# Kernel tuning notes

Measured on AMD Instinct MI355X. Metric: run time of the kernel, lower is better.

## Reference

```python
import jax, jax.numpy as jnp
import numpy as np

N = 50000
E = 800000
F_IN = 128
HID = 64
HEADS = 4
P = 16384


def setup_inputs() -> dict:
    key = jax.random.key(0)
    ks = jax.random.split(key, 20)
    s = 0.05
    inp = {
        'x': jax.random.normal(ks[0], (N, F_IN), jnp.float32),
        'edge_src': jax.random.randint(ks[1], (E,), 0, N, jnp.int32),
        'edge_dst': jax.random.randint(ks[2], (E,), 0, N, jnp.int32),
        'edge_attr': jax.random.uniform(ks[3], (E, 1), jnp.float32),
        'pair_indices': jax.random.randint(ks[4], (P, 2), 0, N, jnp.int32),
        # conv1: in=F_IN, heads=4, out=HID, edge_dim=1
        'W1': jax.random.normal(ks[5], (F_IN, HEADS * HID), jnp.float32) * s,
        'We1': jax.random.normal(ks[6], (1, HEADS * HID), jnp.float32) * s,
        'as1': jax.random.normal(ks[7], (HEADS, HID), jnp.float32) * s,
        'ad1': jax.random.normal(ks[8], (HEADS, HID), jnp.float32) * s,
        'ae1': jax.random.normal(ks[9], (HEADS, HID), jnp.float32) * s,
        'b1': jnp.zeros((HEADS * HID,), jnp.float32),
        # conv2: in=4*HID, heads=1, out=HID
        'W2': jax.random.normal(ks[10], (HEADS * HID, HID), jnp.float32) * s,
        'We2': jax.random.normal(ks[11], (1, HID), jnp.float32) * s,
        'as2': jax.random.normal(ks[12], (1, HID), jnp.float32) * s,
        'ad2': jax.random.normal(ks[13], (1, HID), jnp.float32) * s,
        'ae2': jax.random.normal(ks[14], (1, HID), jnp.float32) * s,
        'b2': jnp.zeros((HID,), jnp.float32),
        'Wlin': jax.random.normal(ks[15], (2 * HID, 1), jnp.float32) * s,
        'blin': jnp.zeros((1,), jnp.float32),
    }
    return inp


def gat_conv(x, src, dst, edge_attr, W, We, att_src, att_dst, att_edge, bias, heads, C):
    """PyG GATConv (add_self_loops=True, fill_value='mean', negative_slope=0.2, eval mode)."""
    n = x.shape[0]
    # self-loop edge_attr = mean of incoming edge attrs per node
    deg = jax.ops.segment_sum(jnp.ones_like(dst, dtype=edge_attr.dtype), dst, num_segments=n)
    loop_attr = jax.ops.segment_sum(edge_attr, dst, num_segments=n) / jnp.maximum(deg, 1.0)[:, None]
    loop = jnp.arange(n, dtype=src.dtype)
    src_f = jnp.concatenate([src, loop])
    dst_f = jnp.concatenate([dst, loop])
    ea = jnp.concatenate([edge_attr, loop_attr], axis=0)  # [E+N, 1]
    h = (x @ W).reshape(n, heads, C)                      # [N, H, C]
    a_src = (h * att_src).sum(-1)                         # [N, H]
    a_dst = (h * att_dst).sum(-1)
    e = (ea @ We).reshape(-1, heads, C)                   # [E+N, H, C]
    a_edge = (e * att_edge).sum(-1)                       # [E+N, H]
    alpha = jax.nn.leaky_relu(a_src[src_f] + a_dst[dst_f] + a_edge, 0.2)
    amax = jax.ops.segment_max(alpha, dst_f, num_segments=n)
    ex = jnp.exp(alpha - amax[dst_f])
    denom = jax.ops.segment_sum(ex, dst_f, num_segments=n)
    w = ex / denom[dst_f]                                 # segment softmax over dst
    msg = h[src_f] * w[..., None]                         # [E+N, H, C]
    out = jax.ops.segment_sum(msg, dst_f, num_segments=n) # [N, H, C]
    return out.reshape(n, heads * C) + bias


def reference(x, edge_src, edge_dst, edge_attr, pair_indices,
              W1, We1, as1, ad1, ae1, b1,
              W2, We2, as2, ad2, ae2, b2, Wlin, blin):
    # dropout is identity in eval mode
    h1 = jax.nn.elu(gat_conv(x, edge_src, edge_dst, edge_attr,
                             W1, We1, as1, ad1, ae1, b1, HEADS, HID))
    h2 = gat_conv(h1, edge_src, edge_dst, edge_attr,
                  W2, We2, as2, ad2, ae2, b2, 1, HID)
    d1 = h2[pair_indices[:, 0]]
    d2 = h2[pair_indices[:, 1]]
    pf = jnp.concatenate([d1, d2], axis=1)                # [P, 2*HID]
    return jax.nn.sigmoid(pf @ Wlin + blin).reshape(-1)
```

## Files before the change

### kernel.cpp

```cpp
#include <hip/hip_runtime.h>
#include <hip/hip_fp16.h>
#include <math.h>

typedef __attribute__((ext_vector_type(8))) short short8;
typedef __attribute__((ext_vector_type(4))) float floatx4;
typedef __attribute__((ext_vector_type(2))) float float2v;

__device__ __forceinline__ unsigned short f2bf(float f){
  unsigned int x = __float_as_uint(f);
  unsigned int r = x + 0x7fff + ((x >> 16) & 1);
  return (unsigned short)(r >> 16);
}
__device__ __forceinline__ unsigned char f2fp8(float v){
  int pk = __builtin_amdgcn_cvt_pk_fp8_f32(v, 0.f, 0, false);
  return (unsigned char)(pk & 0xff);
}
__device__ __forceinline__ float wsumf(float v){
#pragma unroll
  for (int o = 32; o; o >>= 1) v += __shfl_xor(v, o, 64);
  return v;
}

__global__ __launch_bounds__(256) void k_count(const int* __restrict__ dst,
    const float* __restrict__ eattr, unsigned long long* __restrict__ degp,
    int* __restrict__ rank, int E, int N){
  int e = blockIdx.x * 256 + threadIdx.x;
  if (e >= E) return;
  int b = blockIdx.x & 7;
  int d = dst[e];
  unsigned long long add = (1ull << 40) |
      (unsigned long long)(eattr[e] * 16777216.0f);
  unsigned long long old = atomicAdd(&degp[(size_t)b * N + d], add);
  rank[e] = (int)(old >> 40);
}

__global__ __launch_bounds__(256) void k_scan1(const unsigned long long* __restrict__ degp,
    int* __restrict__ row_ptr, int* __restrict__ bsum, int n){
  __shared__ int sm[2][256];
  int tid = threadIdx.x, gid = blockIdx.x * 256 + tid;
  int v = 0;
  if (gid < n){
#pragma unroll
    for (int b = 0; b < 8; b++) v += (int)(degp[(size_t)b * n + gid] >> 40);
  }
  sm[0][tid] = v; __syncthreads();
  int pin = 0;
  for (int off = 1; off < 256; off <<= 1){
    int t = sm[pin][tid];
    if (tid >= off) t += sm[pin][tid - off];
    sm[pin ^ 1][tid] = t; pin ^= 1; __syncthreads();
  }
  int incl = sm[pin][tid];
  if (gid < n) row_ptr[gid] = incl - v;
  if (tid == 255) bsum[blockIdx.x] = incl;
}

__global__ __launch_bounds__(256) void k_scan2(const int* __restrict__ bsum,
    int* __restrict__ bofs, int nb){
  __shared__ int sm[2][256];
  int tid = threadIdx.x;
  int v = (tid < nb) ? bsum[tid] : 0;
  sm[0][tid] = v; __syncthreads();
  int pin = 0;
  for (int off = 1; off < 256; off <<= 1){
    int t = sm[pin][tid];
    if (tid >= off) t += sm[pin][tid - off];
    sm[pin ^ 1][tid] = t; pin ^= 1; __syncthreads();
  }
  bofs[tid] = sm[pin][tid] - v;
}

__global__ __launch_bounds__(256) void k_scan3(int* __restrict__ row_ptr,
    const int* __restrict__ bofs, const unsigned long long* __restrict__ degp,
    float* __restrict__ lattr, int* __restrict__ base, int n, int E){
  int gid = blockIdx.x * 256 + threadIdx.x;
  if (gid >= n) return;
  int rp = row_ptr[gid] + bofs[gid >> 8];
  row_ptr[gid] = rp;
  const unsigned long long M40 = (1ull << 40) - 1;
  int cum = 0; float s = 0.f;
  int bb[8];
#pragma unroll
  for (int b = 0; b < 8; b++){
    unsigned long long p = degp[(size_t)b * n + gid];
    bb[b] = rp + cum;
    cum += (int)(p >> 40);
    s += (float)(p & M40);
  }
  lattr[gid] = (s * (1.0f / 16777216.0f)) / fmaxf((float)cum, 1.0f);
  int4* bp = (int4*)(base + (size_t)gid * 8);
  bp[0] = make_int4(bb[0], bb[1], bb[2], bb[3]);
  bp[1] = make_int4(bb[4], bb[5], bb[6], bb[7]);
  if (gid == 0) row_ptr[n] = E;
}

__global__ __launch_bounds__(256) void k_scatter(const int* __restrict__ src,
    const int* __restrict__ dst, const float* __restrict__ eattr,
    const int* __restrict__ rank, const int* __restrict__ base,
    int2* __restrict__ csr, int E){
  int e = blockIdx.x * 256 + threadIdx.x;
  if (e >= E) return;
  int b = blockIdx.x & 7;
  int d = dst[e];
  int pos = base[(size_t)d * 8 + b] + rank[e];
  csr[pos] = make_int2(src[e], __float_as_int(eattr[e]));
}

__global__ void k_prep(const float* __restrict__ W1, const float* __restrict__ as1,
    const float* __restrict__ ad1, const float* __restrict__ W2,
    const float* __restrict__ as2, const float* __restrict__ ad2,
    const float* __restrict__ We1, const float* __restrict__ ae1,
    const float* __restrict__ We2, const float* __restrict__ ae2,
    unsigned short* __restrict__ W1p, unsigned short* __restrict__ W2p,
    float* __restrict__ ce){
  int b = blockIdx.x, lane = threadIdx.x;
  if (b < 68){
    int nt = b >> 2, kc = b & 3;
    int col = lane & 15, krow = kc * 32 + (lane >> 4) * 8;
    unsigned short tmp[8];
    if (nt < 16){
#pragma unroll
      for (int j = 0; j < 8; j++) tmp[j] = f2bf(W1[(size_t)(krow + j) * 256 + nt * 16 + col]);
    } else {
#pragma unroll
      for (int j = 0; j < 8; j++){
        float v = 0.f;
        if (col < 8){
          const float* av = (col < 4) ? as1 : ad1;
          int h = col & 3;
          for (int c = 0; c < 64; c++)
            v += W1[(size_t)(krow + j) * 256 + h * 64 + c] * av[h * 64 + c];
        }
        tmp[j] = f2bf(v);
      }
    }
    unsigned short* dstp = W1p + (((size_t)nt * 4 + kc) * 64 + lane) * 8;
    *(ushort4*)(dstp)     = make_ushort4(tmp[0], tmp[1], tmp[2], tmp[3]);
    *(ushort4*)(dstp + 4) = make_ushort4(tmp[4], tmp[5], tmp[6], tmp[7]);
  } else if (b < 108){
    int bb = b - 68;
    int nt = bb >> 3, kc = bb & 7;
    int col = lane & 15, krow = kc * 32 + (lane >> 4) * 8;
    unsigned short tmp[8];
    if (nt < 4){
#pragma unroll
      for (int j = 0; j < 8; j++) tmp[j] = f2bf(W2[(size_t)(krow + j) * 64 + nt * 16 + col]);
    } else {
#pragma unroll
      for (int j = 0; j < 8; j++){
        float v = 0.f;
        if (col < 2){
          const float* av = (col == 0) ? as2 : ad2;
          for (int c = 0; c < 64; c++)
            v += W2[(size_t)(krow + j) * 64 + c] * av[c];
        }
        tmp[j] = f2bf(v);
      }
    }
    unsigned short* dstp = W2p + (((size_t)nt * 8 + kc) * 64 + lane) * 8;
    *(ushort4*)(dstp)     = make_ushort4(tmp[0], tmp[1], tmp[2], tmp[3]);
    *(ushort4*)(dstp + 4) = make_ushort4(tmp[4], tmp[5], tmp[6], tmp[7]);
  } else {
    float p0 = We1[lane]       * ae1[lane];
    float p1 = We1[64 + lane]  * ae1[64 + lane];
    float p2 = We1[128 + lane] * ae1[128 + lane];
    float p3 = We1[192 + lane] * ae1[192 + lane];
    float p4 = We2[lane]       * ae2[lane];
    p0 = wsumf(p0); p1 = wsumf(p1); p2 = wsumf(p2); p3 = wsumf(p3); p4 = wsumf(p4);
    if (lane == 0){ ce[0] = p0; ce[1] = p1; ce[2] = p2; ce[3] = p3; ce[4] = p4; }
  }
}

__global__ __launch_bounds__(256) void k_gemm1_att(const float* __restrict__ A,
    const unsigned short* __restrict__ Bp, unsigned char* __restrict__ h1f8,
    float* __restrict__ asrc, float* __restrict__ adst, int M){
  constexpr int K = 128, NKC = 4;
  __shared__ unsigned short Bs[256 * K];
  {
    const uint4* srcp = (const uint4*)Bp;
    uint4* dstp = (uint4*)Bs;
    for (int i = threadIdx.x; i < 4096; i += 256) dstp[i] = srcp[i];
  }
  __syncthreads();
  int wave = threadIdx.x >> 6, lane = threadIdx.x & 63;
  int quad = lane >> 4, col = lane & 15;
  int r0 = (blockIdx.x * 4 + wave) * 16;
  int rowc = min(r0 + col, M - 1);
  short8 af[NKC], sf[NKC];
#pragma unroll
  for (int kc = 0; kc < NKC; kc++){
    float4 a0 = *(const float4*)(A + (size_t)rowc * K + kc * 32 + quad * 8);
    float4 a1 = *(const float4*)(A + (size_t)rowc * K + kc * 32 + quad * 8 + 4);
    short8 t;
    t[0] = (short)f2bf(a0.x); t[1] = (short)f2bf(a0.y);
    t[2] = (short)f2bf(a0.z); t[3] = (short)f2bf(a0.w);
    t[4] = (short)f2bf(a1.x); t[5] = (short)f2bf(a1.y);
    t[6] = (short)f2bf(a1.z); t[7] = (short)f2bf(a1.w);
    af[kc] = t;
    sf[kc] = *(const short8*)(Bp + (((size_t)16 * 4 + kc) * 64 + lane) * 8);
  }
  floatx4 acc[17];
#pragma unroll
  for (int nt = 0; nt < 17; nt++) acc[nt] = (floatx4){0.f, 0.f, 0.f, 0.f};
#pragma unroll
  for (int kc = 0; kc < NKC; kc++){
#pragma unroll
    for (int nt = 0; nt < 16; nt++){
      short8 bfv = *(const short8*)(&Bs[((nt * NKC + kc) * 64 + lane) * 8]);
      acc[nt] = __builtin_amdgcn_mfma_f32_16x16x32_bf16(af[kc], bfv, acc[nt], 0, 0, 0);
    }
    acc[16] = __builtin_amdgcn_mfma_f32_16x16x32_bf16(af[kc], sf[kc], acc[16], 0, 0, 0);
  }
#pragma unroll
  for (int nt = 0; nt < 16; nt++){
#pragma unroll
    for (int i = 0; i < 4; i++){
      int r = r0 + quad * 4 + i;
      if (r < M) h1f8[(size_t)r * 256 + nt * 16 + col] = f2fp8(acc[nt][i]);
    }
  }
#pragma unroll
  for (int i = 0; i < 4; i++){
    int r = r0 + quad * 4 + i;
    if (r < M){
      float v = acc[16][i];
      if (col < 4)      asrc[(size_t)r * 4 + col] = v;
      else if (col < 8) adst[(size_t)r * 4 + (col - 4)] = v;
    }
  }
}

__global__ __launch_bounds__(256) void k_gemm2_att(const unsigned short* __restrict__ A,
    const unsigned short* __restrict__ Bp, unsigned char* __restrict__ h2f8,
    float* __restrict__ asrc, float* __restrict__ adst, int M){
  constexpr int K = 256, NKC = 8;
  __shared__ unsigned short Bs[64 * K];
  {
    const uint4* srcp = (const uint4*)Bp;
    uint4* dstp = (uint4*)Bs;
    for (int i = threadIdx.x; i < 2048; i += 256) dstp[i] = srcp[i];
  }
  __syncthreads();
  int wave = threadIdx.x >> 6, lane = threadIdx.x & 63;
  int quad = lane >> 4, col = lane & 15;
  int r0 = (blockIdx.x * 4 + wave) * 16;
  int rowc = min(r0 + col, M - 1);
  short8 af[NKC], sf[NKC];
#pragma unroll
  for (int kc = 0; kc < NKC; kc++){
    af[kc] = *(const short8*)(A + (size_t)rowc * K + kc * 32 + quad * 8);
    sf[kc] = *(const short8*)(Bp + (((size_t)4 * 8 + kc) * 64 + lane) * 8);
  }
  floatx4 acc[5];
#pragma unroll
  for (int nt = 0; nt < 5; nt++) acc[nt] = (floatx4){0.f, 0.f, 0.f, 0.f};
#pragma unroll
  for (int kc = 0; kc < NKC; kc++){
#pragma unroll
    for (int nt = 0; nt < 4; nt++){
      short8 bfv = *(const short8*)(&Bs[((nt * NKC + kc) * 64 + lane) * 8]);
      acc[nt] = __builtin_amdgcn_mfma_f32_16x16x32_bf16(af[kc], bfv, acc[nt], 0, 0, 0);
    }
    acc[4] = __builtin_amdgcn_mfma_f32_16x16x32_bf16(af[kc], sf[kc], acc[4], 0, 0, 0);
  }
#pragma unroll
  for (int nt = 0; nt < 4; nt++){
#pragma unroll
    for (int i = 0; i < 4; i++){
      int r = r0 + quad * 4 + i;
      if (r < M) h2f8[(size_t)r * 64 + nt * 16 + col] = f2fp8(acc[nt][i]);
    }
  }
#pragma unroll
  for (int i = 0; i < 4; i++){
    int r = r0 + quad * 4 + i;
    if (r < M){
      float v = acc[4][i];
      if (col == 0)      asrc[r] = v;
      else if (col == 1) adst[r] = v;
    }
  }
}

__global__ __launch_bounds__(256) void k_gat1(
    const int* __restrict__ row_ptr, const int2* __restrict__ csr,
    const float* __restrict__ lattr,
    const float* __restrict__ a_src, const float* __restrict__ a_dst,
    const float* __restrict__ ce, const unsigned char* __restrict__ hpre,
    const float* __restrict__ bias, unsigned short* __restrict__ hout, int n){
  int node = blockIdx.x * 4 + (threadIdx.x >> 6);
  if (node >= n) return;
  int lane = threadIdx.x & 63;
  int q = lane >> 4, lsub = lane & 15, hq = lsub >> 2;
  int start = row_ptr[node], deg = row_ptr[node + 1] - start;
  float4 as4 = *(const float4*)(a_src + (size_t)node * 4);
  float4 ad4 = *(const float4*)(a_dst + (size_t)node * 4);
  float4 ce4 = *(const float4*)ce;
  float la = lattr[node];
  float asvh = hq == 0 ? as4.x : hq == 1 ? as4.y : hq == 2 ? as4.z : as4.w;
  float advh = hq == 0 ? ad4.x : hq == 1 ? ad4.y : hq == 2 ? ad4.z : ad4.w;
  float ceh  = hq == 0 ? ce4.x : hq == 1 ? ce4.y : hq == 2 ? ce4.z : ce4.w;
  float2v acc2[8];
#pragma unroll
  for (int k = 0; k < 8; k++) acc2[k] = (float2v){0.f, 0.f};
  float dn = 0.f;
  if (q == 0){
    float aself = asvh + advh + la * ceh;
    aself = aself > 0.f ? aself : 0.2f * aself;
    float wself = __expf(aself);
    dn = wself;
    uint4 u = *(const uint4*)(hpre + (size_t)node * 256 + lsub * 16);
    float2v w2 = (float2v){wself, wself};
    unsigned uu[4] = {u.x, u.y, u.z, u.w};
#pragma unroll
    for (int j = 0; j < 4; j++){
      acc2[2 * j]     = w2 * __builtin_amdgcn_cvt_pk_f32_fp8((int)uu[j], false);
      acc2[2 * j + 1] = w2 * __builtin_amdgcn_cvt_pk_f32_fp8((int)uu[j], true);
    }
  }
  for (int e = q; e < deg; e += 8){
    bool vB = (e + 4) < deg;
    int2 seA = csr[start + e];
    int2 seB = csr[start + (vB ? e + 4 : e)];
    float aA = a_src[(size_t)seA.x * 4 + hq] + advh + __int_as_float(seA.y) * ceh;
    aA = aA > 0.f ? aA : 0.2f * aA;
    float wA = __expf(aA);
    float aB = a_src[(size_t)seB.x * 4 + hq] + advh + __int_as_float(seB.y) * ceh;
    aB = aB > 0.f ? aB : 0.2f * aB;
    float wB = vB ? __expf(aB) : 0.f;
    uint4 uA = *(const uint4*)(hpre + (size_t)seA.x * 256 + lsub * 16);
    uint4 uB = *(const uint4*)(hpre + (size_t)seB.x * 256 + lsub * 16);
    dn += wA + wB;
    float2v wA2 = (float2v){wA, wA}, wB2 = (float2v){wB, wB};
    unsigned ua[4] = {uA.x, uA.y, uA.z, uA.w};
    unsigned ub[4] = {uB.x, uB.y, uB.z, uB.w};
#pragma unroll
    for (int j = 0; j < 4; j++){
      acc2[2 * j]     += wA2 * __builtin_amdgcn_cvt_pk_f32_fp8((int)ua[j], false);
      acc2[2 * j + 1] += wA2 * __builtin_amdgcn_cvt_pk_f32_fp8((int)ua[j], true);
      acc2[2 * j]     += wB2 * __builtin_amdgcn_cvt_pk_f32_fp8((int)ub[j], false);
      acc2[2 * j + 1] += wB2 * __builtin_amdgcn_cvt_pk_f32_fp8((int)ub[j], true);
    }
  }
  dn += __shfl_xor(dn, 16, 64);
  dn += __shfl_xor(dn, 32, 64);
#pragma unroll
  for (int k = 0; k < 8; k++){
    acc2[k].x += __shfl_xor(acc2[k].x, 16, 64);
    acc2[k].x += __shfl_xor(acc2[k].x, 32, 64);
    acc2[k].y += __shfl_xor(acc2[k].y, 16, 64);
    acc2[k].y += __shfl_xor(acc2[k].y, 32, 64);
  }
  if (q == 0){
    float inv = 1.f / dn;
    float bb[16];
#pragma unroll
    for (int j = 0; j < 4; j++){
      float4 b4 = *(const float4*)(bias + lsub * 16 + j * 4);
      bb[j * 4 + 0] = b4.x; bb[j * 4 + 1] = b4.y;
      bb[j * 4 + 2] = b4.z; bb[j * 4 + 3] = b4.w;
    }
    unsigned short o[16];
#pragma unroll
    for (int k = 0; k < 16; k++){
      float av = (k & 1) ? acc2[k >> 1].y : acc2[k >> 1].x;
      float v = av * inv + bb[k];
      v = v > 0.f ? v : (__expf(v) - 1.f);
      o[k] = f2bf(v);
    }
    unsigned short* op = hout + (size_t)node * 256 + lsub * 16;
    *(uint4*)(op)     = *(uint4*)(o);
    *(uint4*)(op + 8) = *(uint4*)(o + 8);
  }
}

__global__ __launch_bounds__(256) void k_gat2(
    const int* __restrict__ row_ptr, const int2* __restrict__ csr,
    const float* __restrict__ lattr,
    const float* __restrict__ a_src, const float* __restrict__ a_dst,
    const float* __restrict__ ce, const unsigned char* __restrict__ hpre,
    const float* __restrict__ bias, const float* __restrict__ Wlin,
    float* __restrict__ s1v, float* __restrict__ s2v, int n){
  int node = blockIdx.x * 4 + (threadIdx.x >> 6);
  if (node >= n) return;
  int lane = threadIdx.x & 63;
  int slot = lane >> 3, lsub = lane & 7;
  int start = row_ptr[node], deg = row_ptr[node + 1] - start;
  float adn = a_dst[node], c = ce[4];
  float2v acc2[4];
#pragma unroll
  for (int k = 0; k < 4; k++) acc2[k] = (float2v){0.f, 0.f};
  float dn = 0.f;
  if (slot == 0){
    float aself = a_src[node] + adn + lattr[node] * c;
    aself = aself > 0.f ? aself : 0.2f * aself;
    float wself = __expf(aself);
    dn = wself;
    uint2 u = *(const uint2*)(hpre + (size_t)node * 64 + lsub * 8);
    float2v w2 = (float2v){wself, wself};
    unsigned uu[2] = {u.x, u.y};
#pragma unroll
    for (int j = 0; j < 2; j++){
      acc2[2 * j]     = w2 * __builtin_amdgcn_cvt_pk_f32_fp8((int)uu[j], false);
      acc2[2 * j + 1] = w2 * __builtin_amdgcn_cvt_pk_f32_fp8((int)uu[j], true);
    }
  }
  for (int e = slot; e < deg; e += 16){
    bool vB = (e + 8) < deg;
    int2 seA = csr[start + e];
    int2 seB = csr[start + (vB ? e + 8 : e)];
    float aA = a_src[seA.x] + adn + __int_as_float(seA.y) * c;
    aA = aA > 0.f ? aA : 0.2f * aA;
    float wA = __expf(aA);
    float aB = a_src[seB.x] + adn + __int_as_float(seB.y) * c;
    aB = aB > 0.f ? aB : 0.2f * aB;
    float wB = vB ? __expf(aB) : 0.f;
    uint2 uA = *(const uint2*)(hpre + (size_t)seA.x * 64 + lsub * 8);
    uint2 uB = *(const uint2*)(hpre + (size_t)seB.x * 64 + lsub * 8);
    dn += wA + wB;
    float2v wA2 = (float2v){wA, wA}, wB2 = (float2v){wB, wB};
    unsigned ua[2] = {uA.x, uA.y};
    unsigned ub[2] = {uB.x, uB.y};
#pragma unroll
    for (int j = 0; j < 2; j++){
      acc2[2 * j]     += wA2 * __builtin_amdgcn_cvt_pk_f32_fp8((int)ua[j], false);
      acc2[2 * j + 1] += wA2 * __builtin_amdgcn_cvt_pk_f32_fp8((int)ua[j], true);
      acc2[2 * j]     += wB2 * __builtin_amdgcn_cvt_pk_f32_fp8((int)ub[j], false);
      acc2[2 * j + 1] += wB2 * __builtin_amdgcn_cvt_pk_f32_fp8((int)ub[j], true);
    }
  }
#pragma unroll
  for (int o = 8; o < 64; o <<= 1){
    dn += __shfl_xor(dn, o, 64);
#pragma unroll
    for (int k = 0; k < 4; k++){
      acc2[k].x += __shfl_xor(acc2[k].x, o, 64);
      acc2[k].y += __shfl_xor(acc2[k].y, o, 64);
    }
  }
  float inv = 1.f / dn;
  float t1 = 0.f, t2 = 0.f;
#pragma unroll
  for (int k = 0; k < 8; k++){
    float av = (k & 1) ? acc2[k >> 1].y : acc2[k >> 1].x;
    float v = av * inv + bias[lsub * 8 + k];
    t1 += v * Wlin[lsub * 8 + k];
    t2 += v * Wlin[64 + lsub * 8 + k];
  }
#pragma unroll
  for (int o = 1; o < 8; o <<= 1){
    t1 += __shfl_xor(t1, o, 64);
    t2 += __shfl_xor(t2, o, 64);
  }
  if (lane == 0){ s1v[node] = t1; s2v[node] = t2; }
}

__global__ __launch_bounds__(256) void k_pairs(const int* __restrict__ pairs,
    const float* __restrict__ s1v, const float* __restrict__ s2v,
    const float* __restrict__ blin, float* __restrict__ out, int P){
  int p = blockIdx.x * 256 + threadIdx.x;
  if (p >= P) return;
  int i = pairs[2 * p], j = pairs[2 * p + 1];
  float x = s1v[i] + s2v[j] + blin[0];
  out[p] = 1.f / (1.f + __expf(-x));
}

extern "C" void kernel_launch(void* const* d_in, const int* in_sizes, int n_in,
                              void* d_out, int out_size, void* d_ws, size_t ws_size,
                              hipStream_t stream) {
  const float* x     = (const float*)d_in[0];
  const int*   esrc  = (const int*)  d_in[1];
  const int*   edst  = (const int*)  d_in[2];
  const float* eattr = (const float*)d_in[3];
  const int*   pairs = (const int*)  d_in[4];
  const float* W1    = (const float*)d_in[5];
  const float* We1   = (const float*)d_in[6];
  const float* as1   = (const float*)d_in[7];
  const float* ad1   = (const float*)d_in[8];
  const float* ae1   = (const float*)d_in[9];
  const float* b1    = (const float*)d_in[10];
  const float* W2    = (const float*)d_in[11];
  const float* We2   = (const float*)d_in[12];
  const float* as2   = (const float*)d_in[13];
  const float* ad2   = (const float*)d_in[14];
  const float* ae2   = (const float*)d_in[15];
  const float* b2    = (const float*)d_in[16];
  const float* Wlin  = (const float*)d_in[17];
  const float* blin  = (const float*)d_in[18];
  float* out = (float*)d_out;

  const int N = in_sizes[0] / 128;
  const int E = in_sizes[1];
  const int P = in_sizes[4] / 2;

  char* w = (char*)d_ws;
  size_t off = 0;
  auto alloc = [&](size_t bytes) -> size_t {
    size_t r = off; off = (off + bytes + 255) & ~(size_t)255; return r;
  };
  size_t o_degp   = alloc((size_t)N * 64);
  size_t zero_end = off;
  size_t o_rank   = alloc((size_t)E * 4);
  size_t o_rowptr = alloc((size_t)(N + 1) * 4);
  size_t o_bsum   = alloc(1024);
  size_t o_bofs   = alloc(1024);
  size_t o_lattr  = alloc((size_t)N * 4);
  size_t o_base   = alloc((size_t)N * 32);
  size_t o_csr    = alloc((size_t)E * 8);
  size_t o_asrc1  = alloc((size_t)N * 16);
  size_t o_adst1  = alloc((size_t)N * 16);
  size_t o_asrc2  = alloc((size_t)N * 4);
  size_t o_adst2  = alloc((size_t)N * 4);
  size_t o_ce     = alloc(32);
  size_t o_s1     = alloc((size_t)N * 4);
  size_t o_s2     = alloc((size_t)N * 4);
  size_t o_W1p    = alloc((size_t)17 * 4 * 64 * 8 * 2);
  size_t o_W2p    = alloc((size_t)5 * 8 * 64 * 8 * 2);
  size_t o_h1f8   = alloc((size_t)N * 256);
  size_t o_h1b    = alloc((size_t)N * 256 * 2);
  size_t o_h2f8   = alloc((size_t)N * 64);
  (void)ws_size;

  unsigned long long* degp = (unsigned long long*)(w + o_degp);
  int*   rank   = (int*)  (w + o_rank);
  int*   rowptr = (int*)  (w + o_rowptr);
  int*   bsum   = (int*)  (w + o_bsum);
  int*   bofs   = (int*)  (w + o_bofs);
  float* lattr  = (float*)(w + o_lattr);
  int*   base   = (int*)  (w + o_base);
  int2*  csr    = (int2*) (w + o_csr);
  float* asrc1  = (float*)(w + o_asrc1);
  float* adst1  = (float*)(w + o_adst1);
  float* asrc2  = (float*)(w + o_asrc2);
  float* adst2  = (float*)(w + o_adst2);
  float* ce     = (float*)(w + o_ce);
  float* s1v    = (float*)(w + o_s1);
  float* s2v    = (float*)(w + o_s2);
  unsigned short* W1p = (unsigned short*)(w + o_W1p);
  unsigned short* W2p = (unsigned short*)(w + o_W2p);
  unsigned char*  h1f8 = (unsigned char*)(w + o_h1f8);
  unsigned short* h1b  = (unsigned short*)(w + o_h1b);
  unsigned char*  h2f8 = (unsigned char*)(w + o_h2f8);

  hipMemsetAsync(w, 0, zero_end, stream);

  int ebl = (E + 255) / 256;
  int nbl = (N + 255) / 256;
  int wbl = (N + 3) / 4;

  k_count<<<ebl, 256, 0, stream>>>(edst, eattr, degp, rank, E, N);
  k_scan1<<<nbl, 256, 0, stream>>>(degp, rowptr, bsum, N);
  k_scan2<<<1, 256, 0, stream>>>(bsum, bofs, nbl);
  k_scan3<<<nbl, 256, 0, stream>>>(rowptr, bofs, degp, lattr, base, N, E);
  k_scatter<<<ebl, 256, 0, stream>>>(esrc, edst, eattr, rank, base, csr, E);

  k_prep<<<109, 64, 0, stream>>>(W1, as1, ad1, W2, as2, ad2,
                                 We1, ae1, We2, ae2, W1p, W2p, ce);

  k_gemm1_att<<<(N + 63) / 64, 256, 0, stream>>>(x, W1p, h1f8, asrc1, adst1, N);
  k_gat1<<<wbl, 256, 0, stream>>>(rowptr, csr, lattr, asrc1, adst1, ce,
                                  h1f8, b1, h1b, N);
  k_gemm2_att<<<(N + 63) / 64, 256, 0, stream>>>(h1b, W2p, h2f8, asrc2, adst2, N);
  k_gat2<<<wbl, 256, 0, stream>>>(rowptr, csr, lattr, asrc2, adst2, ce,
                                  h2f8, b2, Wlin, s1v, s2v, N);
  k_pairs<<<(P + 255) / 256, 256, 0, stream>>>(pairs, s1v, s2v, blin, out, P);
}
```

Baseline: 280.2 us.

## Fold layer-2 projection and final linear into per-node scalars, drop GEMM2

Since conv2 has a single head and its output only feeds a linear readout, W2 is folded with att_src, att_dst and the two halves of Wlin into a 256x4 matrix. The first aggregation kernel now emits four scalars per node instead of a bf16 256-wide hidden row. The second GEMM and the 64-wide fp8 gather in layer 2 are removed, and the second aggregation uses 8 lanes per node over float4 scalars. The bias contribution is applied afterwards via precomputed constants, which changes rounding order and skips the bf16/fp8 quantisation of layer-2 features.

```diff
diff --git a/kernel.cpp b/kernel.cpp
--- a/kernel.cpp
+++ b/kernel.cpp
@@ -111,7 +111,8 @@
     const float* __restrict__ as2, const float* __restrict__ ad2,
     const float* __restrict__ We1, const float* __restrict__ ae1,
     const float* __restrict__ We2, const float* __restrict__ ae2,
-    unsigned short* __restrict__ W1p, unsigned short* __restrict__ W2p,
+    const float* __restrict__ b2, const float* __restrict__ Wlin,
+    unsigned short* __restrict__ W1p, float4* __restrict__ w2v,
     float* __restrict__ ce){
   int b = blockIdx.x, lane = threadIdx.x;
   if (b < 68){
@@ -137,37 +138,31 @@
     unsigned short* dstp = W1p + (((size_t)nt * 4 + kc) * 64 + lane) * 8;
     *(ushort4*)(dstp)     = make_ushort4(tmp[0], tmp[1], tmp[2], tmp[3]);
     *(ushort4*)(dstp + 4) = make_ushort4(tmp[4], tmp[5], tmp[6], tmp[7]);
-  } else if (b < 108){
-    int bb = b - 68;
-    int nt = bb >> 3, kc = bb & 7;
-    int col = lane & 15, krow = kc * 32 + (lane >> 4) * 8;
-    unsigned short tmp[8];
-    if (nt < 4){
-#pragma unroll
-      for (int j = 0; j < 8; j++) tmp[j] = f2bf(W2[(size_t)(krow + j) * 64 + nt * 16 + col]);
-    } else {
-#pragma unroll
-      for (int j = 0; j < 8; j++){
-        float v = 0.f;
-        if (col < 2){
-          const float* av = (col == 0) ? as2 : ad2;
-          for (int c = 0; c < 64; c++)
-            v += W2[(size_t)(krow + j) * 64 + c] * av[c];
-        }
-        tmp[j] = f2bf(v);
-      }
-    }
-    unsigned short* dstp = W2p + (((size_t)nt * 8 + kc) * 64 + lane) * 8;
-    *(ushort4*)(dstp)     = make_ushort4(tmp[0], tmp[1], tmp[2], tmp[3]);
-    *(ushort4*)(dstp + 4) = make_ushort4(tmp[4], tmp[5], tmp[6], tmp[7]);
+  } else if (b < 72){
+    int k = (b - 68) * 64 + lane;
+    float4 a = make_float4(0.f, 0.f, 0.f, 0.f);
+    for (int c = 0; c < 64; c++){
+      float wv = W2[(size_t)k * 64 + c];
+      a.x += wv * as2[c];
+      a.y += wv * ad2[c];
+      a.z += wv * Wlin[c];
+      a.w += wv * Wlin[64 + c];
+    }
+    w2v[k] = a;
   } else {
     float p0 = We1[lane]       * ae1[lane];
     float p1 = We1[64 + lane]  * ae1[64 + lane];
     float p2 = We1[128 + lane] * ae1[128 + lane];
     float p3 = We1[192 + lane] * ae1[192 + lane];
     float p4 = We2[lane]       * ae2[lane];
+    float c1 = b2[lane] * Wlin[lane];
+    float c2 = b2[lane] * Wlin[64 + lane];
     p0 = wsumf(p0); p1 = wsumf(p1); p2 = wsumf(p2); p3 = wsumf(p3); p4 = wsumf(p4);
-    if (lane == 0){ ce[0] = p0; ce[1] = p1; ce[2] = p2; ce[3] = p3; ce[4] = p4; }
+    c1 = wsumf(c1); c2 = wsumf(c2);
+    if (lane == 0){
+      ce[0] = p0; ce[1] = p1; ce[2] = p2; ce[3] = p3; ce[4] = p4;
+      ce[5] = c1; ce[6] = c2;
+    }
   }
 }
 
@@ -230,64 +225,13 @@
   }
 }
 
-__global__ __launch_bounds__(256) void k_gemm2_att(const unsigned short* __restrict__ A,
-    const unsigned short* __restrict__ Bp, unsigned char* __restrict__ h2f8,
-    float* __restrict__ asrc, float* __restrict__ adst, int M){
-  constexpr int K = 256, NKC = 8;
-  __shared__ unsigned short Bs[64 * K];
-  {
-    const uint4* srcp = (const uint4*)Bp;
-    uint4* dstp = (uint4*)Bs;
-    for (int i = threadIdx.x; i < 2048; i += 256) dstp[i] = srcp[i];
-  }
-  __syncthreads();
-  int wave = threadIdx.x >> 6, lane = threadIdx.x & 63;
-  int quad = lane >> 4, col = lane & 15;
-  int r0 = (blockIdx.x * 4 + wave) * 16;
-  int rowc = min(r0 + col, M - 1);
-  short8 af[NKC], sf[NKC];
-#pragma unroll
-  for (int kc = 0; kc < NKC; kc++){
-    af[kc] = *(const short8*)(A + (size_t)rowc * K + kc * 32 + quad * 8);
-    sf[kc] = *(const short8*)(Bp + (((size_t)4 * 8 + kc) * 64 + lane) * 8);
-  }
-  floatx4 acc[5];
-#pragma unroll
-  for (int nt = 0; nt < 5; nt++) acc[nt] = (floatx4){0.f, 0.f, 0.f, 0.f};
-#pragma unroll
-  for (int kc = 0; kc < NKC; kc++){
-#pragma unroll
-    for (int nt = 0; nt < 4; nt++){
-      short8 bfv = *(const short8*)(&Bs[((nt * NKC + kc) * 64 + lane) * 8]);
-      acc[nt] = __builtin_amdgcn_mfma_f32_16x16x32_bf16(af[kc], bfv, acc[nt], 0, 0, 0);
-    }
-    acc[4] = __builtin_amdgcn_mfma_f32_16x16x32_bf16(af[kc], sf[kc], acc[4], 0, 0, 0);
-  }
-#pragma unroll
-  for (int nt = 0; nt < 4; nt++){
-#pragma unroll
-    for (int i = 0; i < 4; i++){
-      int r = r0 + quad * 4 + i;
-      if (r < M) h2f8[(size_t)r * 64 + nt * 16 + col] = f2fp8(acc[nt][i]);
-    }
-  }
-#pragma unroll
-  for (int i = 0; i < 4; i++){
-    int r = r0 + quad * 4 + i;
-    if (r < M){
-      float v = acc[4][i];
-      if (col == 0)      asrc[r] = v;
-      else if (col == 1) adst[r] = v;
-    }
-  }
-}
-
 __global__ __launch_bounds__(256) void k_gat1(
     const int* __restrict__ row_ptr, const int2* __restrict__ csr,
     const float* __restrict__ lattr,
     const float* __restrict__ a_src, const float* __restrict__ a_dst,
     const float* __restrict__ ce, const unsigned char* __restrict__ hpre,
-    const float* __restrict__ bias, unsigned short* __restrict__ hout, int n){
+    const float* __restrict__ bias, const float4* __restrict__ w2v,
+    float4* __restrict__ upd, int n){
   int node = blockIdx.x * 4 + (threadIdx.x >> 6);
   if (node >= n) return;
   int lane = threadIdx.x & 63;
@@ -360,99 +304,63 @@
       bb[j * 4 + 0] = b4.x; bb[j * 4 + 1] = b4.y;
       bb[j * 4 + 2] = b4.z; bb[j * 4 + 3] = b4.w;
     }
-    unsigned short o[16];
+    float d0 = 0.f, d1 = 0.f, d2 = 0.f, d3 = 0.f;
 #pragma unroll
     for (int k = 0; k < 16; k++){
       float av = (k & 1) ? acc2[k >> 1].y : acc2[k >> 1].x;
       float v = av * inv + bb[k];
       v = v > 0.f ? v : (__expf(v) - 1.f);
-      o[k] = f2bf(v);
-    }
-    unsigned short* op = hout + (size_t)node * 256 + lsub * 16;
-    *(uint4*)(op)     = *(uint4*)(o);
-    *(uint4*)(op + 8) = *(uint4*)(o + 8);
+      float4 wv = w2v[lsub * 16 + k];
+      d0 += v * wv.x; d1 += v * wv.y; d2 += v * wv.z; d3 += v * wv.w;
+    }
+#pragma unroll
+    for (int o = 1; o < 16; o <<= 1){
+      d0 += __shfl_xor(d0, o, 64);
+      d1 += __shfl_xor(d1, o, 64);
+      d2 += __shfl_xor(d2, o, 64);
+      d3 += __shfl_xor(d3, o, 64);
+    }
+    if (lsub == 0) upd[node] = make_float4(d0, d1, d2, d3);
   }
 }
 
 __global__ __launch_bounds__(256) void k_gat2(
     const int* __restrict__ row_ptr, const int2* __restrict__ csr,
-    const float* __restrict__ lattr,
-    const float* __restrict__ a_src, const float* __restrict__ a_dst,
-    const float* __restrict__ ce, const unsigned char* __restrict__ hpre,
-    const float* __restrict__ bias, const float* __restrict__ Wlin,
+    const float* __restrict__ lattr, const float4* __restrict__ upd,
+    const float* __restrict__ ce,
     float* __restrict__ s1v, float* __restrict__ s2v, int n){
-  int node = blockIdx.x * 4 + (threadIdx.x >> 6);
+  int node = blockIdx.x * 32 + (threadIdx.x >> 3);
   if (node >= n) return;
-  int lane = threadIdx.x & 63;
-  int slot = lane >> 3, lsub = lane & 7;
+  int lane8 = threadIdx.x & 7;
   int start = row_ptr[node], deg = row_ptr[node + 1] - start;
-  float adn = a_dst[node], c = ce[4];
-  float2v acc2[4];
-#pragma unroll
-  for (int k = 0; k < 4; k++) acc2[k] = (float2v){0.f, 0.f};
-  float dn = 0.f;
-  if (slot == 0){
-    float aself = a_src[node] + adn + lattr[node] * c;
-    aself = aself > 0.f ? aself : 0.2f * aself;
-    float wself = __expf(aself);
-    dn = wself;
-    uint2 u = *(const uint2*)(hpre + (size_t)node * 64 + lsub * 8);
-    float2v w2 = (float2v){wself, wself};
-    unsigned uu[2] = {u.x, u.y};
-#pragma unroll
-    for (int j = 0; j < 2; j++){
-      acc2[2 * j]     = w2 * __builtin_amdgcn_cvt_pk_f32_fp8((int)uu[j], false);
-      acc2[2 * j + 1] = w2 * __builtin_amdgcn_cvt_pk_f32_fp8((int)uu[j], true);
-    }
-  }
-  for (int e = slot; e < deg; e += 16){
-    bool vB = (e + 8) < deg;
-    int2 seA = csr[start + e];
-    int2 seB = csr[start + (vB ? e + 8 : e)];
-    float aA = a_src[seA.x] + adn + __int_as_float(seA.y) * c;
-    aA = aA > 0.f ? aA : 0.2f * aA;
-    float wA = __expf(aA);
-    float aB = a_src[seB.x] + adn + __int_as_float(seB.y) * c;
-    aB = aB > 0.f ? aB : 0.2f * aB;
-    float wB = vB ? __expf(aB) : 0.f;
-    uint2 uA = *(const uint2*)(hpre + (size_t)seA.x * 64 + lsub * 8);
-    uint2 uB = *(const uint2*)(hpre + (size_t)seB.x * 64 + lsub * 8);
-    dn += wA + wB;
-    float2v wA2 = (float2v){wA, wA}, wB2 = (float2v){wB, wB};
-    unsigned ua[2] = {uA.x, uA.y};
-    unsigned ub[2] = {uB.x, uB.y};
-#pragma unroll
-    for (int j = 0; j < 2; j++){
-      acc2[2 * j]     += wA2 * __builtin_amdgcn_cvt_pk_f32_fp8((int)ua[j], false);
-      acc2[2 * j + 1] += wA2 * __builtin_amdgcn_cvt_pk_f32_fp8((int)ua[j], true);
-      acc2[2 * j]     += wB2 * __builtin_amdgcn_cvt_pk_f32_fp8((int)ub[j], false);
-      acc2[2 * j + 1] += wB2 * __builtin_amdgcn_cvt_pk_f32_fp8((int)ub[j], true);
-    }
-  }
-#pragma unroll
-  for (int o = 8; o < 64; o <<= 1){
+  float4 own = upd[node];
+  float ad = own.y, c = ce[4];
+  float t1 = 0.f, t2 = 0.f, dn = 0.f;
+  if (lane8 == 0){
+    float a = own.x + ad + lattr[node] * c;
+    a = a > 0.f ? a : 0.2f * a;
+    float w = __expf(a);
+    dn = w; t1 = w * own.z; t2 = w * own.w;
+  }
+  for (int e = lane8; e < deg; e += 8){
+    int2 se = csr[start + e];
+    float4 o = upd[se.x];
+    float a = o.x + ad + __int_as_float(se.y) * c;
+    a = a > 0.f ? a : 0.2f * a;
+    float w = __expf(a);
+    dn += w; t1 += w * o.z; t2 += w * o.w;
+  }
+#pragma unroll
+  for (int o = 1; o < 8; o <<= 1){
     dn += __shfl_xor(dn, o, 64);
-#pragma unroll
-    for (int k = 0; k < 4; k++){
-      acc2[k].x += __shfl_xor(acc2[k].x, o, 64);
-      acc2[k].y += __shfl_xor(acc2[k].y, o, 64);
-    }
-  }
-  float inv = 1.f / dn;
-  float t1 = 0.f, t2 = 0.f;
-#pragma unroll
-  for (int k = 0; k < 8; k++){
-    float av = (k & 1) ? acc2[k >> 1].y : acc2[k >> 1].x;
-    float v = av * inv + bias[lsub * 8 + k];
-    t1 += v * Wlin[lsub * 8 + k];
-    t2 += v * Wlin[64 + lsub * 8 + k];
-  }
-#pragma unroll
-  for (int o = 1; o < 8; o <<= 1){
     t1 += __shfl_xor(t1, o, 64);
     t2 += __shfl_xor(t2, o, 64);
   }
-  if (lane == 0){ s1v[node] = t1; s2v[node] = t2; }
+  if (lane8 == 0){
+    float inv = 1.f / dn;
+    s1v[node] = t1 * inv + ce[5];
+    s2v[node] = t2 * inv + ce[6];
+  }
 }
 
 __global__ __launch_bounds__(256) void k_pairs(const int* __restrict__ pairs,
@@ -509,16 +417,13 @@
   size_t o_csr    = alloc((size_t)E * 8);
   size_t o_asrc1  = alloc((size_t)N * 16);
   size_t o_adst1  = alloc((size_t)N * 16);
-  size_t o_asrc2  = alloc((size_t)N * 4);
-  size_t o_adst2  = alloc((size_t)N * 4);
-  size_t o_ce     = alloc(32);
+  size_t o_upd    = alloc((size_t)N * 16);
+  size_t o_ce     = alloc(64);
   size_t o_s1     = alloc((size_t)N * 4);
   size_t o_s2     = alloc((size_t)N * 4);
   size_t o_W1p    = alloc((size_t)17 * 4 * 64 * 8 * 2);
-  size_t o_W2p    = alloc((size_t)5 * 8 * 64 * 8 * 2);
+  size_t o_w2v    = alloc(256 * 16);
   size_t o_h1f8   = alloc((size_t)N * 256);
-  size_t o_h1b    = alloc((size_t)N * 256 * 2);
-  size_t o_h2f8   = alloc((size_t)N * 64);
   (void)ws_size;
 
   unsigned long long* degp = (unsigned long long*)(w + o_degp);
@@ -531,16 +436,13 @@
   int2*  csr    = (int2*) (w + o_csr);
   float* asrc1  = (float*)(w + o_asrc1);
   float* adst1  = (float*)(w + o_adst1);
-  float* asrc2  = (float*)(w + o_asrc2);
-  float* adst2  = (float*)(w + o_adst2);
+  float4* upd   = (float4*)(w + o_upd);
   float* ce     = (float*)(w + o_ce);
   float* s1v    = (float*)(w + o_s1);
   float* s2v    = (float*)(w + o_s2);
   unsigned short* W1p = (unsigned short*)(w + o_W1p);
-  unsigned short* W2p = (unsigned short*)(w + o_W2p);
-  unsigned char*  h1f8 = (unsigned char*)(w + o_h1f8);
-  unsigned short* h1b  = (unsigned short*)(w + o_h1b);
-  unsigned char*  h2f8 = (unsigned char*)(w + o_h2f8);
+  float4* w2v   = (float4*)(w + o_w2v);
+  unsigned char* h1f8 = (unsigned char*)(w + o_h1f8);
 
   hipMemsetAsync(w, 0, zero_end, stream);
 
@@ -554,14 +456,13 @@
   k_scan3<<<nbl, 256, 0, stream>>>(rowptr, bofs, degp, lattr, base, N, E);
   k_scatter<<<ebl, 256, 0, stream>>>(esrc, edst, eattr, rank, base, csr, E);
 
-  k_prep<<<109, 64, 0, stream>>>(W1, as1, ad1, W2, as2, ad2,
-                                 We1, ae1, We2, ae2, W1p, W2p, ce);
+  k_prep<<<73, 64, 0, stream>>>(W1, as1, ad1, W2, as2, ad2,
+                                We1, ae1, We2, ae2, b2, Wlin, W1p, w2v, ce);
 
   k_gemm1_att<<<(N + 63) / 64, 256, 0, stream>>>(x, W1p, h1f8, asrc1, adst1, N);
   k_gat1<<<wbl, 256, 0, stream>>>(rowptr, csr, lattr, asrc1, adst1, ce,
-                                  h1f8, b1, h1b, N);
-  k_gemm2_att<<<(N + 63) / 64, 256, 0, stream>>>(h1b, W2p, h2f8, asrc2, adst2, N);
-  k_gat2<<<wbl, 256, 0, stream>>>(rowptr, csr, lattr, asrc2, adst2, ce,
-                                  h2f8, b2, Wlin, s1v, s2v, N);
+                                  h1f8, b1, w2v, upd, N);
+  k_gat2<<<(N + 31) / 32, 256, 0, stream>>>(rowptr, csr, lattr, upd, ce,
+                                            s1v, s2v, N);
   k_pairs<<<(P + 255) / 256, 256, 0, stream>>>(pairs, s1v, s2v, blin, out, P);
 }
```

Measured after the change: 279.4 us. About the same (-0.3%).
